# Kernel tuning notes

Measured on AMD Instinct MI355X. Metric: run time of the kernel, lower is better.

The kernel has to match this reference:

```python
import jax, jax.numpy as jnp
import numpy as np

N, E, F_IN, C, H = 50000, 800000, 256, 64, 2  # nodes, edges, in-feat, per-head dim, heads
NEG_SLOPE_ATT = 0.2   # GATConv leaky_relu slope
NEG_SLOPE = 0.01      # F.leaky_relu default
BN_EPS = 1e-5


def setup_inputs() -> dict:
    key = jax.random.key(0)
    ks = jax.random.split(key, 10)
    x = jax.random.normal(ks[0], (N, F_IN), dtype=jnp.float32)
    edge_index = jax.random.randint(ks[1], (2, E), 0, N, dtype=jnp.int32)
    # GATConv params
    W = jax.random.normal(ks[2], (F_IN, H * C), dtype=jnp.float32) / np.sqrt(F_IN)
    att_src = jax.random.normal(ks[3], (H, C), dtype=jnp.float32) / np.sqrt(C)
    att_dst = jax.random.normal(ks[4], (H, C), dtype=jnp.float32) / np.sqrt(C)
    conv_bias = jnp.zeros((H * C,), dtype=jnp.float32)
    # fc1: in = hidden*2*2 = 256, out = hidden = 64
    fc1_w = jax.random.normal(ks[5], (H * C * 2, C), dtype=jnp.float32) / np.sqrt(H * C * 2)
    fc1_b = jnp.zeros((C,), dtype=jnp.float32)
    bn_gamma = jnp.ones((C,), dtype=jnp.float32)
    bn_beta = jnp.zeros((C,), dtype=jnp.float32)
    bn_mean = jnp.zeros((C,), dtype=jnp.float32)
    bn_var = jnp.ones((C,), dtype=jnp.float32)
    fc2_w = jax.random.normal(ks[6], (C, 3), dtype=jnp.float32) / np.sqrt(C)
    fc2_b = jnp.zeros((3,), dtype=jnp.float32)
    return {"x": x, "edge_index": edge_index, "W": W, "att_src": att_src,
            "att_dst": att_dst, "conv_bias": conv_bias, "fc1_w": fc1_w, "fc1_b": fc1_b,
            "bn_gamma": bn_gamma, "bn_beta": bn_beta, "bn_mean": bn_mean,
            "bn_var": bn_var, "fc2_w": fc2_w, "fc2_b": fc2_b}


def gat_conv(x, edge_index, W, att_src, att_dst, bias):
    # Project: [N, H, C]
    h = (x @ W).reshape(N, H, C)
    a_s = jnp.einsum('nhc,hc->nh', h, att_src)  # [N, H]
    a_d = jnp.einsum('nhc,hc->nh', h, att_dst)
    # add self-loops (PyG default)
    loops = jnp.arange(N, dtype=edge_index.dtype)
    src = jnp.concatenate([edge_index[0], loops])
    dst = jnp.concatenate([edge_index[1], loops])
    e = jax.nn.leaky_relu(a_s[src] + a_d[dst], NEG_SLOPE_ATT)  # [E+N, H]
    # segment softmax over incoming edges of each dst node
    m = jax.ops.segment_max(e, dst, num_segments=N)
    e_exp = jnp.exp(e - m[dst])
    denom = jax.ops.segment_sum(e_exp, dst, num_segments=N)
    alpha = e_exp / denom[dst]  # [E+N, H]
    msg = h[src] * alpha[:, :, None]  # [E+N, H, C]
    out = jax.ops.segment_sum(msg, dst, num_segments=N)  # [N, H, C]
    return out.reshape(N, H * C) + bias


def reference(x, edge_index, W, att_src, att_dst, conv_bias, fc1_w, fc1_b,
              bn_gamma, bn_beta, bn_mean, bn_var, fc2_w, fc2_b):
    # eval mode: dropout = identity, BN uses running stats
    h = gat_conv(x, edge_index, W, att_src, att_dst, conv_bias)
    h = jax.nn.leaky_relu(h, NEG_SLOPE)
    edge_rep = jnp.concatenate([h[edge_index[0]], h[edge_index[1]]], axis=1)  # [E, 256]
    y = edge_rep @ fc1_w + fc1_b
    y = (y - bn_mean) * jax.lax.rsqrt(bn_var + BN_EPS) * bn_gamma + bn_beta
    y = jax.nn.leaky_relu(y, NEG_SLOPE)
    return y @ fc2_w + fc2_b  # [E, 3]
```

## Files before the change

### kernel.cpp

```cpp
#include <hip/hip_runtime.h>
#include <hip/hip_bf16.h>

#define N_NODES 50000
#define N_EDGES 800000
#define F_IN    256
#define C_DIM   64
#define HC      128
#define NPG     6250
#define NBB     32
#define NBLK    196
#define XW_BLOCKS   3125
#define HIST_BLOCKS 256

typedef __attribute__((ext_vector_type(8))) short bf16x8;
typedef __attribute__((ext_vector_type(4))) float f32x4;

static constexpr size_t OFF_HBF   = 0;
static constexpr size_t OFF_H2    = 12800000;
static constexpr size_t OFF_AB    = 25600000;
static constexpr size_t OFF_AS    = 38400000;
static constexpr size_t OFF_AD    = 38800000;
static constexpr size_t OFF_OFFS  = 39200000;
static constexpr size_t OFF_TOT   = 39400064;
static constexpr size_t OFF_PART  = 39800064;
static constexpr size_t OFF_CSR2  = 39801088;
static constexpr size_t OFF_WT    = 46201088;
static constexpr size_t OFF_FC1T  = 46266624;
static constexpr size_t OFF_SCALE = 46299392;
static constexpr size_t OFF_CC    = 46299904;
static constexpr size_t OFF_FC2M  = 46300416;
static constexpr size_t OFF_BCNT  = 46302464;
static constexpr size_t OFF_BASE  = 52702464;

__device__ __forceinline__ float2 bf2(unsigned u) {
    float2 r;
    r.x = __uint_as_float(u << 16);
    r.y = __uint_as_float(u & 0xffff0000u);
    return r;
}
__device__ __forceinline__ unsigned short f2bf(float f) {
    unsigned u = __float_as_uint(f);
    return (unsigned short)((u + 0x7fffu + ((u >> 16) & 1u)) >> 16);
}
__device__ __forceinline__ short f2bf_s(float f) {
    __hip_bfloat16 h = __float2bfloat16(f);
    return *reinterpret_cast<short*>(&h);
}

__global__ __launch_bounds__(256) void k_prep(const float* __restrict__ W,
                                              const float* __restrict__ fc1,
                                              const float* __restrict__ fc1_b,
                                              const float* __restrict__ gamma,
                                              const float* __restrict__ beta,
                                              const float* __restrict__ mean,
                                              const float* __restrict__ var,
                                              const float* __restrict__ fc2_w,
                                              unsigned short* __restrict__ Wt,
                                              unsigned short* __restrict__ fc1t,
                                              float* __restrict__ scale,
                                              float* __restrict__ cc,
                                              unsigned short* __restrict__ fc2m) {
    int id = blockIdx.x * 256 + threadIdx.x;
    if (id < 32768) {
        int n = id >> 8, k = id & 255;
        Wt[id] = f2bf(W[k * HC + n]);
    }
    int id2 = id - 32768;
    if (id2 >= 0 && id2 < 16384) {
        int j = id2 >> 7, q = id2 & 127;
        int L = q >> 1, b = q & 1;
        int kch = 32 * (L >> 4) + (L & 15) + 16 * b;
        float v = (j < 64) ? fc1[kch * 64 + j] : fc1[(128 + kch) * 64 + (j - 64)];
        fc1t[id2] = f2bf(v);
    }
    int id3 = id - (32768 + 16384);
    if (id3 >= 0 && id3 < 128) {
        int jj = id3 & 63;
        float s = gamma[jj] * rsqrtf(var[jj] + 1e-5f);
        scale[id3] = s;
        cc[id3] = (id3 < 64) ? 0.f : (fc1_b[jj] - mean[jj]) * s + beta[jj];
    }
    int id4 = id - (32768 + 16384 + 128);
    if (id4 >= 0 && id4 < 1024) {
        int kk = id4 >> 9, rem = id4 & 511;
        int lane = rem >> 3, j = rem & 7;
        int q  = kk * 16 + (lane >> 4) * 4 + (j >> 1);
        int ch = 32 * (q >> 4) + (q & 15) + 16 * (j & 1);
        int col = lane & 15;
        float v = (col < 3) ? fc2_w[ch * 3 + col] : 0.f;
        fc2m[id4] = f2bf(v);
    }
}

__global__ __launch_bounds__(256, 4) void k_front(const float* __restrict__ x,
                                                  const unsigned short* __restrict__ Wt,
                                                  const float* __restrict__ att_src,
                                                  const float* __restrict__ att_dst,
                                                  unsigned* __restrict__ h_p,
                                                  float* __restrict__ as_,
                                                  float* __restrict__ ad_,
                                                  const int* __restrict__ dst,
                                                  int* __restrict__ bcnt) {
    __shared__ int smem[6464];
    const int t = threadIdx.x;

    if (blockIdx.x < HIST_BLOCKS) {
        int* hist = smem;
        const int bid = blockIdx.x;
        const int g  = bid & 7;
        const int bi = bid >> 3;
        const int lo = g * NPG, hi = lo + NPG;
        for (int j = t; j < NPG; j += 256) hist[j] = 0;
        __syncthreads();
        const int4* d4 = (const int4*)dst + bi * 6250;
#pragma unroll 1
        for (int it = 0; it < 25; ++it) {
            int idx = it * 256 + t;
            if (idx < 6250) {
                int4 d = d4[idx];
                if (d.x >= lo && d.x < hi) atomicAdd(&hist[d.x - lo], 1);
                if (d.y >= lo && d.y < hi) atomicAdd(&hist[d.y - lo], 1);
                if (d.z >= lo && d.z < hi) atomicAdd(&hist[d.z - lo], 1);
                if (d.w >= lo && d.w < hi) atomicAdd(&hist[d.w - lo], 1);
            }
        }
        __syncthreads();
        int* row = bcnt + (size_t)(g * NBB + bi) * NPG;
        for (int j = t; j < NPG; j += 256) row[j] = hist[j];
        return;
    }

    float* xs  = (float*)smem;
    float* sAs = (float*)(smem + 4096);
    float* sAd = sAs + 32;
    const int v    = t >> 6;
    const int lane = t & 63;
    const int c16  = lane & 15;
    const int kg   = lane >> 4;
    const int r0   = (blockIdx.x - HIST_BLOCKS) * 16;
    if (t < 32) { sAs[t] = 0.f; sAd[t] = 0.f; }
    {
        const float4* xsrc = (const float4*)(x + (size_t)r0 * F_IN);
        float4* xsl = (float4*)xs;
#pragma unroll
        for (int it = 0; it < 4; ++it) {
            int cidx = it * 256 + t;
            int rl = cidx >> 6, j = cidx & 63;
            float4 val = xsrc[cidx];
            xsl[rl * 64 + (j ^ rl)] = val;
        }
    }
    const int cf0 = 2 * v, cf1 = 2 * v + 1;
    bf16x8 wf0[8], wf1[8];
#pragma unroll
    for (int kk = 0; kk < 8; ++kk) {
        wf0[kk] = *(const bf16x8*)(Wt + (size_t)(cf0 * 16 + c16) * 256 + kk * 32 + kg * 8);
        wf1[kk] = *(const bf16x8*)(Wt + (size_t)(cf1 * 16 + c16) * 256 + kk * 32 + kg * 8);
    }
    __syncthreads();

    f32x4 acc0 = {}, acc1 = {};
#pragma unroll
    for (int kk = 0; kk < 8; ++kk) {
        int j0 = kk * 8 + kg * 2;
        float4 a0 = *(const float4*)(xs + (size_t)(c16 * 64 + (j0 ^ c16)) * 4);
        float4 a1 = *(const float4*)(xs + (size_t)(c16 * 64 + ((j0 + 1) ^ c16)) * 4);
        float fv[8] = {a0.x, a0.y, a0.z, a0.w, a1.x, a1.y, a1.z, a1.w};
        bf16x8 ahi, alo;
#pragma unroll
        for (int q = 0; q < 8; ++q) {
            unsigned u = __float_as_uint(fv[q]);
            float hval = __uint_as_float(u & 0xffff0000u);
            float d = fv[q] - hval;
            ahi[q] = (short)(u >> 16);
            alo[q] = (short)(__float_as_uint(d) >> 16);
        }
        acc0 = __builtin_amdgcn_mfma_f32_16x16x32_bf16(alo, wf0[kk], acc0, 0, 0, 0);
        acc0 = __builtin_amdgcn_mfma_f32_16x16x32_bf16(ahi, wf0[kk], acc0, 0, 0, 0);
        acc1 = __builtin_amdgcn_mfma_f32_16x16x32_bf16(alo, wf1[kk], acc1, 0, 0, 0);
        acc1 = __builtin_amdgcn_mfma_f32_16x16x32_bf16(ahi, wf1[kk], acc1, 0, 0, 0);
    }
#pragma unroll
    for (int i = 0; i < 4; ++i) {
        int row = r0 + kg * 4 + i;
        unsigned pu = (unsigned)f2bf(acc0[i]) | ((unsigned)f2bf(acc1[i]) << 16);
        h_p[(size_t)row * 64 + v * 16 + c16] = pu;
    }
    float ws0 = att_src[cf0 * 16 + c16], ws1 = att_src[cf1 * 16 + c16];
    float wd0 = att_dst[cf0 * 16 + c16], wd1 = att_dst[cf1 * 16 + c16];
    float pas[4], pad[4];
#pragma unroll
    for (int i = 0; i < 4; ++i) {
        pas[i] = acc0[i] * ws0 + acc1[i] * ws1;
        pad[i] = acc0[i] * wd0 + acc1[i] * wd1;
    }
#pragma unroll
    for (int m = 1; m < 16; m <<= 1) {
#pragma unroll
        for (int i = 0; i < 4; ++i) {
            pas[i] += __shfl_xor(pas[i], m, 64);
            pad[i] += __shfl_xor(pad[i], m, 64);
        }
    }
    const int head = v >> 1;
    if (c16 == 0) {
#pragma unroll
        for (int i = 0; i < 4; ++i) {
            atomicAdd(&sAs[(kg * 4 + i) * 2 + head], pas[i]);
            atomicAdd(&sAd[(kg * 4 + i) * 2 + head], pad[i]);
        }
    }
    __syncthreads();
    if (t < 32) {
        int row = t >> 1, hd = t & 1;
        as_[(r0 + row) * 2 + hd] = sAs[row * 2 + hd];
        ad_[(r0 + row) * 2 + hd] = sAd[row * 2 + hd];
    }
}

__global__ void k_tot_part(const int* __restrict__ bcnt, int* __restrict__ tot,
                           int* __restrict__ part) {
    __shared__ int sd[256];
    int n = blockIdx.x * 256 + threadIdx.x;
    int s = 0;
    if (n < N_NODES) {
        int g = n / NPG, ln = n - g * NPG;
        const int* col = bcnt + (size_t)g * NBB * NPG + ln;
#pragma unroll
        for (int bi = 0; bi < NBB; ++bi) s += col[bi * NPG];
        tot[n] = s;
    }
    sd[threadIdx.x] = s;
    __syncthreads();
    for (int off = 128; off > 0; off >>= 1) {
        if (threadIdx.x < off) sd[threadIdx.x] += sd[threadIdx.x + off];
        __syncthreads();
    }
    if (threadIdx.x == 0) part[blockIdx.x] = sd[0];
}

__global__ void k_scan_base(const int* __restrict__ tot, const int* __restrict__ part,
                            const int* __restrict__ bcnt, int* __restrict__ offs,
                            int* __restrict__ base) {
    __shared__ int sp[256];
    __shared__ int sd[256];
    const int t = threadIdx.x;
    int pv = (t < NBLK && t < (int)blockIdx.x) ? part[t] : 0;
    sp[t] = pv;
    __syncthreads();
    for (int off = 128; off > 0; off >>= 1) {
        if (t < off) sp[t] += sp[t + off];
        __syncthreads();
    }
    const int bb = sp[0];
    __syncthreads();
    int i = blockIdx.x * 256 + t;
    int v = (i < N_NODES) ? tot[i] : 0;
    sd[t] = v;
    __syncthreads();
    for (int off = 1; off < 256; off <<= 1) {
        int u = (t >= off) ? sd[t - off] : 0;
        __syncthreads();
        sd[t] += u;
        __syncthreads();
    }
    if (i < N_NODES) {
        int o = bb + sd[t] - v;
        offs[i] = o;
        if (i == N_NODES - 1) offs[N_NODES] = o + v;
        int g = i / NPG, ln = i - g * NPG;
        const int* col = bcnt + (size_t)g * NBB * NPG + ln;
        int* bcol = base + (size_t)g * NBB * NPG + ln;
        int run = o;
#pragma unroll
        for (int bi = 0; bi < NBB; ++bi) {
            bcol[bi * NPG] = run;
            run += col[bi * NPG];
        }
    }
}

__global__ __launch_bounds__(256) void k_scatter(const int* __restrict__ src,
                                                 const int* __restrict__ dst,
                                                 const int* __restrict__ base,
                                                 int2* __restrict__ csr2) {
    __shared__ int cnt[NPG];
    const int g  = blockIdx.x & 7;
    const int bi = blockIdx.x >> 3;
    const int lo = g * NPG, hi = lo + NPG;
    const int* brow = base + (size_t)(g * NBB + bi) * NPG;
    for (int j = threadIdx.x; j < NPG; j += 256) cnt[j] = brow[j];
    __syncthreads();
    const int4* d4 = (const int4*)dst + bi * 6250;
    const int4* s4 = (const int4*)src + bi * 6250;
    const int ebase = bi * 25000;
#pragma unroll 1
    for (int it = 0; it < 25; ++it) {
        int idx = it * 256 + threadIdx.x;
        if (idx < 6250) {
            int4 d = d4[idx];
            int4 s = s4[idx];
            int e = ebase + idx * 4;
            if (d.x >= lo && d.x < hi) { int p = atomicAdd(&cnt[d.x - lo], 1); csr2[p] = make_int2(s.x, e);     }
            if (d.y >= lo && d.y < hi) { int p = atomicAdd(&cnt[d.y - lo], 1); csr2[p] = make_int2(s.y, e + 1); }
            if (d.z >= lo && d.z < hi) { int p = atomicAdd(&cnt[d.z - lo], 1); csr2[p] = make_int2(s.z, e + 2); }
            if (d.w >= lo && d.w < hi) { int p = atomicAdd(&cnt[d.w - lo], 1); csr2[p] = make_int2(s.w, e + 3); }
        }
    }
}

__global__ __launch_bounds__(256) void k_agg(const unsigned* __restrict__ h_p,
                                             const float* __restrict__ as_,
                                             const float* __restrict__ ad_,
                                             const int* __restrict__ offs,
                                             const int2* __restrict__ csr2,
                                             const float* __restrict__ conv_bias,
                                             unsigned* __restrict__ h2_p) {
    const int n    = blockIdx.x * 4 + (threadIdx.x >> 6);
    const int lane = threadIdx.x & 63;
    const int ql   = lane & 15;
    const int q    = lane >> 4;
    const int hd   = ql >> 3;
    const float adn = ad_[n * 2 + hd];
    const uint4* h4 = (const uint4*)h_p;
    float a[8] = {};
    float accw = 0.f;
    const int beg = offs[n], end = offs[n + 1];
    int i = beg + q;
    for (; i + 4 < end; i += 8) {
        int s0 = csr2[i].x;
        int s1 = csr2[i + 4].x;
        uint4 u0 = h4[(unsigned)(s0 * 16 + ql)];
        uint4 u1 = h4[(unsigned)(s1 * 16 + ql)];
        float l0 = as_[s0 * 2 + hd] + adn;
        float l1 = as_[s1 * 2 + hd] + adn;
        l0 = fmaxf(l0, 0.2f * l0);
        l1 = fmaxf(l1, 0.2f * l1);
        float w0 = __expf(l0), w1 = __expf(l1);
        float2 t;
        t = bf2(u0.x); a[0] += w0 * t.x; a[1] += w0 * t.y;
        t = bf2(u0.y); a[2] += w0 * t.x; a[3] += w0 * t.y;
        t = bf2(u0.z); a[4] += w0 * t.x; a[5] += w0 * t.y;
        t = bf2(u0.w); a[6] += w0 * t.x; a[7] += w0 * t.y;
        t = bf2(u1.x); a[0] += w1 * t.x; a[1] += w1 * t.y;
        t = bf2(u1.y); a[2] += w1 * t.x; a[3] += w1 * t.y;
        t = bf2(u1.z); a[4] += w1 * t.x; a[5] += w1 * t.y;
        t = bf2(u1.w); a[6] += w1 * t.x; a[7] += w1 * t.y;
        accw += w0 + w1;
    }
    if (i < end) {
        int s0 = csr2[i].x;
        uint4 u0 = h4[(unsigned)(s0 * 16 + ql)];
        float l0 = as_[s0 * 2 + hd] + adn;
        l0 = fmaxf(l0, 0.2f * l0);
        float w0 = __expf(l0);
        float2 t;
        t = bf2(u0.x); a[0] += w0 * t.x; a[1] += w0 * t.y;
        t = bf2(u0.y); a[2] += w0 * t.x; a[3] += w0 * t.y;
        t = bf2(u0.z); a[4] += w0 * t.x; a[5] += w0 * t.y;
        t = bf2(u0.w); a[6] += w0 * t.x; a[7] += w0 * t.y;
        accw += w0;
    }
#pragma unroll
    for (int m = 16; m < 64; m <<= 1) {
#pragma unroll
        for (int j = 0; j < 8; ++j) a[j] += __shfl_xor(a[j], m, 64);
        accw += __shfl_xor(accw, m, 64);
    }
    if (q == 0) {
        float es = as_[n * 2 + hd] + adn;
        es = fmaxf(es, 0.2f * es);
        float wsl = __expf(es);
        uint4 un = h4[(unsigned)(n * 16 + ql)];
        float2 t;
        t = bf2(un.x); a[0] += wsl * t.x; a[1] += wsl * t.y;
        t = bf2(un.y); a[2] += wsl * t.x; a[3] += wsl * t.y;
        t = bf2(un.z); a[4] += wsl * t.x; a[5] += wsl * t.y;
        t = bf2(un.w); a[6] += wsl * t.x; a[7] += wsl * t.y;
        accw += wsl;
        float rinv = 1.f / accw;
        unsigned pw[4];
#pragma unroll
        for (int j = 0; j < 4; ++j) {
            int w = 4 * ql + j;
            int c = 32 * (w >> 4) + (w & 15);
            float o0 = a[2 * j] * rinv + conv_bias[c];
            float o1 = a[2 * j + 1] * rinv + conv_bias[c + 16];
            o0 = fmaxf(o0, 0.01f * o0);
            o1 = fmaxf(o1, 0.01f * o1);
            pw[j] = (unsigned)f2bf(o0) | ((unsigned)f2bf(o1) << 16);
        }
        ((uint4*)h2_p)[(unsigned)(n * 16 + ql)] = make_uint4(pw[0], pw[1], pw[2], pw[3]);
    }
}

__global__ __launch_bounds__(256) void k_mfma_uv(const unsigned short* __restrict__ h2,
                                                 const unsigned short* __restrict__ fc1t,
                                                 const float* __restrict__ scale,
                                                 const float* __restrict__ cc,
                                                 unsigned* __restrict__ ab_p) {
    const int w = blockIdx.x * 4 + (threadIdx.x >> 6);
    if (w >= N_NODES / 16) return;
    const int lane = threadIdx.x & 63;
    const int c16  = lane & 15;
    const int kg   = lane >> 4;
    const int r0   = w * 16;
    const unsigned short* arow = h2 + (size_t)(r0 + c16) * HC + kg * 8;
    bf16x8 af[4];
#pragma unroll
    for (int kk = 0; kk < 4; ++kk) af[kk] = *(const bf16x8*)(arow + kk * 32);
    f32x4 acc[8] = {};
#pragma unroll
    for (int kk = 0; kk < 4; ++kk) {
        const unsigned short* wp = fc1t + c16 * HC + kk * 32 + kg * 8;
#pragma unroll
        for (int cf = 0; cf < 8; ++cf) {
            bf16x8 b = *(const bf16x8*)(wp + cf * 16 * HC);
            acc[cf] = __builtin_amdgcn_mfma_f32_16x16x32_bf16(af[kk], b, acc[cf], 0, 0, 0);
        }
    }
#pragma unroll
    for (int cf = 0; cf < 8; cf += 2) {
        int j0 = cf * 16 + c16, j1 = j0 + 16;
        float s0 = scale[j0], s1 = scale[j1];
        float q0 = cc[j0],    q1 = cc[j1];
#pragma unroll
        for (int i = 0; i < 4; ++i) {
            int row = r0 + kg * 4 + i;
            unsigned pu = (unsigned)f2bf(acc[cf][i] * s0 + q0)
                        | ((unsigned)f2bf(acc[cf + 1][i] * s1 + q1) << 16);
            ab_p[(size_t)row * 64 + (cf >> 1) * 16 + c16] = pu;
        }
    }
}

__device__ __forceinline__ void mk_afrag(uint4 ua, const float* bb, bf16x8& ap) {
    float2 t; float z;
    t = bf2(ua.x);
    z = t.x + bb[0]; z = fmaxf(z, 0.01f * z); ap[0] = f2bf_s(z);
    z = t.y + bb[1]; z = fmaxf(z, 0.01f * z); ap[1] = f2bf_s(z);
    t = bf2(ua.y);
    z = t.x + bb[2]; z = fmaxf(z, 0.01f * z); ap[2] = f2bf_s(z);
    z = t.y + bb[3]; z = fmaxf(z, 0.01f * z); ap[3] = f2bf_s(z);
    t = bf2(ua.z);
    z = t.x + bb[4]; z = fmaxf(z, 0.01f * z); ap[4] = f2bf_s(z);
    z = t.y + bb[5]; z = fmaxf(z, 0.01f * z); ap[5] = f2bf_s(z);
    t = bf2(ua.w);
    z = t.x + bb[6]; z = fmaxf(z, 0.01f * z); ap[6] = f2bf_s(z);
    z = t.y + bb[7]; z = fmaxf(z, 0.01f * z); ap[7] = f2bf_s(z);
}

__global__ __launch_bounds__(256) void k_edge(const int* __restrict__ offs,
                                              const int2* __restrict__ csr2,
                                              const unsigned* __restrict__ ab_p,
                                              const unsigned short* __restrict__ fc2m,
                                              const float* __restrict__ fc2_b,
                                              float* __restrict__ out) {
    const int n    = blockIdx.x * 4 + (threadIdx.x >> 6);
    const int lane = threadIdx.x & 63;
    const int c16  = lane & 15;
    const int kg   = lane >> 4;
    bf16x8 bfr0 = *(const bf16x8*)(fc2m + (size_t)lane * 8);
    bf16x8 bfr1 = *(const bf16x8*)(fc2m + (size_t)(64 + lane) * 8);
    const uint4* abv = (const uint4*)ab_p;
    uint4 ub0 = abv[(unsigned)(n * 16 + 8 + kg)];
    uint4 ub1 = abv[(unsigned)(n * 16 + 12 + kg)];
    float bb0[8], bb1[8];
    {
        float2 t;
        t = bf2(ub0.x); bb0[0] = t.x; bb0[1] = t.y;
        t = bf2(ub0.y); bb0[2] = t.x; bb0[3] = t.y;
        t = bf2(ub0.z); bb0[4] = t.x; bb0[5] = t.y;
        t = bf2(ub0.w); bb0[6] = t.x; bb0[7] = t.y;
        t = bf2(ub1.x); bb1[0] = t.x; bb1[1] = t.y;
        t = bf2(ub1.y); bb1[2] = t.x; bb1[3] = t.y;
        t = bf2(ub1.z); bb1[4] = t.x; bb1[5] = t.y;
        t = bf2(ub1.w); bb1[6] = t.x; bb1[7] = t.y;
    }
    const float ob = (c16 < 3) ? fc2_b[c16] : 0.f;
    const int beg = offs[n], end = offs[n + 1];
    for (int base = beg; base < end; base += 16) {
        int slot = base + c16;
        int2 ce = (slot < end) ? csr2[slot] : make_int2(0, 0);
        uint4 ua0 = abv[(unsigned)(ce.x * 16 + kg)];
        uint4 ua1 = abv[(unsigned)(ce.x * 16 + 4 + kg)];
        bf16x8 ap0, ap1;
        mk_afrag(ua0, bb0, ap0);
        mk_afrag(ua1, bb1, ap1);
        f32x4 acc = {};
        acc = __builtin_amdgcn_mfma_f32_16x16x32_bf16(ap0, bfr0, acc, 0, 0, 0);
        acc = __builtin_amdgcn_mfma_f32_16x16x32_bf16(ap1, bfr1, acc, 0, 0, 0);
#pragma unroll
        for (int i = 0; i < 4; ++i) {
            int eid = __shfl(ce.y, kg * 4 + i, 64);
            if (c16 < 3 && (base + kg * 4 + i) < end)
                out[(size_t)eid * 3 + c16] = acc[i] + ob;
        }
    }
}

extern "C" void kernel_launch(void* const* d_in, const int* in_sizes, int n_in,
                              void* d_out, int out_size, void* d_ws, size_t ws_size,
                              hipStream_t stream) {
    const float* x        = (const float*)d_in[0];
    const int*   ei       = (const int*)d_in[1];
    const float* W        = (const float*)d_in[2];
    const float* att_src  = (const float*)d_in[3];
    const float* att_dst  = (const float*)d_in[4];
    const float* conv_b   = (const float*)d_in[5];
    const float* fc1_w    = (const float*)d_in[6];
    const float* fc1_b    = (const float*)d_in[7];
    const float* gamma    = (const float*)d_in[8];
    const float* beta     = (const float*)d_in[9];
    const float* mean     = (const float*)d_in[10];
    const float* var      = (const float*)d_in[11];
    const float* fc2_w    = (const float*)d_in[12];
    const float* fc2_b    = (const float*)d_in[13];
    float*       out      = (float*)d_out;
    char*        ws       = (char*)d_ws;

    const int* src = ei;
    const int* dst = ei + N_EDGES;

    unsigned*       h_p   = (unsigned*)(ws + OFF_HBF);
    unsigned*       h2_p  = (unsigned*)(ws + OFF_H2);
    unsigned*       ab_p  = (unsigned*)(ws + OFF_AB);
    float*          as_   = (float*)(ws + OFF_AS);
    float*          ad_   = (float*)(ws + OFF_AD);
    int*            offs  = (int*)(ws + OFF_OFFS);
    int*            tot   = (int*)(ws + OFF_TOT);
    int*            part  = (int*)(ws + OFF_PART);
    int2*           csr2  = (int2*)(ws + OFF_CSR2);
    unsigned short* Wt    = (unsigned short*)(ws + OFF_WT);
    unsigned short* fc1t  = (unsigned short*)(ws + OFF_FC1T);
    float*          scale = (float*)(ws + OFF_SCALE);
    float*          cc    = (float*)(ws + OFF_CC);
    unsigned short* fc2m  = (unsigned short*)(ws + OFF_FC2M);
    int*            bcnt  = (int*)(ws + OFF_BCNT);
    int*            base  = (int*)(ws + OFF_BASE);

    k_prep<<<235, 256, 0, stream>>>(W, fc1_w, fc1_b, gamma, beta, mean, var, fc2_w,
                                    Wt, fc1t, scale, cc, fc2m);

    k_front<<<HIST_BLOCKS + XW_BLOCKS, 256, 0, stream>>>(x, Wt, att_src, att_dst,
                                                         h_p, as_, ad_, dst, bcnt);

    k_tot_part <<<NBLK, 256, 0, stream>>>(bcnt, tot, part);
    k_scan_base<<<NBLK, 256, 0, stream>>>(tot, part, bcnt, offs, base);
    k_scatter  <<<8 * NBB, 256, 0, stream>>>(src, dst, base, csr2);

    k_agg    <<<N_NODES / 4, 256, 0, stream>>>(h_p, as_, ad_, offs, csr2, conv_b, h2_p);
    k_mfma_uv<<<(N_NODES / 16 + 3) / 4, 256, 0, stream>>>((const unsigned short*)h2_p, fc1t, scale, cc, ab_p);
    k_edge   <<<N_NODES / 4, 256, 0, stream>>>(offs, csr2, ab_p, fc2m, fc2_b, out);
}
```

Measured before the change: 157.7 us.

## Fuse GAT aggregation with fc1 MFMA projection through shared memory

Merges the aggregation kernel and the per-node fc1 MFMA kernel into one. Each block now handles 16 nodes, four per wavefront processed sequentially, and stages the activated bf16 rows in LDS. After a barrier, each wave computes two 16-column MFMA tiles of the projection. This drops the h2 global round-trip and one launch, but each block gets 4x more serial gather work and a __syncthreads, which lowers parallelism and latency hiding in the gather phase.

```diff
diff --git a/kernel.cpp b/kernel.cpp
--- a/kernel.cpp
+++ b/kernel.cpp
@@ -16,7 +16,6 @@
 typedef __attribute__((ext_vector_type(4))) float f32x4;
 
 static constexpr size_t OFF_HBF   = 0;
-static constexpr size_t OFF_H2    = 12800000;
 static constexpr size_t OFF_AB    = 25600000;
 static constexpr size_t OFF_AS    = 38400000;
 static constexpr size_t OFF_AD    = 38800000;
@@ -309,128 +308,127 @@
     }
 }
 
-__global__ __launch_bounds__(256) void k_agg(const unsigned* __restrict__ h_p,
-                                             const float* __restrict__ as_,
-                                             const float* __restrict__ ad_,
-                                             const int* __restrict__ offs,
-                                             const int2* __restrict__ csr2,
-                                             const float* __restrict__ conv_bias,
-                                             unsigned* __restrict__ h2_p) {
-    const int n    = blockIdx.x * 4 + (threadIdx.x >> 6);
-    const int lane = threadIdx.x & 63;
+__global__ __launch_bounds__(256) void k_agg_uv(const unsigned* __restrict__ h_p,
+                                                const float* __restrict__ as_,
+                                                const float* __restrict__ ad_,
+                                                const int* __restrict__ offs,
+                                                const int2* __restrict__ csr2,
+                                                const float* __restrict__ conv_bias,
+                                                const unsigned short* __restrict__ fc1t,
+                                                const float* __restrict__ scale,
+                                                const float* __restrict__ cc,
+                                                unsigned* __restrict__ ab_p) {
+    __shared__ unsigned lds_h2[16 * 68];
+    const int t    = threadIdx.x;
+    const int v    = t >> 6;
+    const int lane = t & 63;
     const int ql   = lane & 15;
     const int q    = lane >> 4;
     const int hd   = ql >> 3;
-    const float adn = ad_[n * 2 + hd];
+    const int nbase = blockIdx.x * 16;
     const uint4* h4 = (const uint4*)h_p;
-    float a[8] = {};
-    float accw = 0.f;
-    const int beg = offs[n], end = offs[n + 1];
-    int i = beg + q;
-    for (; i + 4 < end; i += 8) {
-        int s0 = csr2[i].x;
-        int s1 = csr2[i + 4].x;
-        uint4 u0 = h4[(unsigned)(s0 * 16 + ql)];
-        uint4 u1 = h4[(unsigned)(s1 * 16 + ql)];
-        float l0 = as_[s0 * 2 + hd] + adn;
-        float l1 = as_[s1 * 2 + hd] + adn;
-        l0 = fmaxf(l0, 0.2f * l0);
-        l1 = fmaxf(l1, 0.2f * l1);
-        float w0 = __expf(l0), w1 = __expf(l1);
-        float2 t;
-        t = bf2(u0.x); a[0] += w0 * t.x; a[1] += w0 * t.y;
-        t = bf2(u0.y); a[2] += w0 * t.x; a[3] += w0 * t.y;
-        t = bf2(u0.z); a[4] += w0 * t.x; a[5] += w0 * t.y;
-        t = bf2(u0.w); a[6] += w0 * t.x; a[7] += w0 * t.y;
-        t = bf2(u1.x); a[0] += w1 * t.x; a[1] += w1 * t.y;
-        t = bf2(u1.y); a[2] += w1 * t.x; a[3] += w1 * t.y;
-        t = bf2(u1.z); a[4] += w1 * t.x; a[5] += w1 * t.y;
-        t = bf2(u1.w); a[6] += w1 * t.x; a[7] += w1 * t.y;
-        accw += w0 + w1;
-    }
-    if (i < end) {
-        int s0 = csr2[i].x;
-        uint4 u0 = h4[(unsigned)(s0 * 16 + ql)];
-        float l0 = as_[s0 * 2 + hd] + adn;
-        l0 = fmaxf(l0, 0.2f * l0);
-        float w0 = __expf(l0);
-        float2 t;
-        t = bf2(u0.x); a[0] += w0 * t.x; a[1] += w0 * t.y;
-        t = bf2(u0.y); a[2] += w0 * t.x; a[3] += w0 * t.y;
-        t = bf2(u0.z); a[4] += w0 * t.x; a[5] += w0 * t.y;
-        t = bf2(u0.w); a[6] += w0 * t.x; a[7] += w0 * t.y;
-        accw += w0;
-    }
-#pragma unroll
-    for (int m = 16; m < 64; m <<= 1) {
-#pragma unroll
-        for (int j = 0; j < 8; ++j) a[j] += __shfl_xor(a[j], m, 64);
-        accw += __shfl_xor(accw, m, 64);
-    }
-    if (q == 0) {
-        float es = as_[n * 2 + hd] + adn;
-        es = fmaxf(es, 0.2f * es);
-        float wsl = __expf(es);
-        uint4 un = h4[(unsigned)(n * 16 + ql)];
-        float2 t;
-        t = bf2(un.x); a[0] += wsl * t.x; a[1] += wsl * t.y;
-        t = bf2(un.y); a[2] += wsl * t.x; a[3] += wsl * t.y;
-        t = bf2(un.z); a[4] += wsl * t.x; a[5] += wsl * t.y;
-        t = bf2(un.w); a[6] += wsl * t.x; a[7] += wsl * t.y;
-        accw += wsl;
-        float rinv = 1.f / accw;
-        unsigned pw[4];
-#pragma unroll
-        for (int j = 0; j < 4; ++j) {
-            int w = 4 * ql + j;
-            int c = 32 * (w >> 4) + (w & 15);
-            float o0 = a[2 * j] * rinv + conv_bias[c];
-            float o1 = a[2 * j + 1] * rinv + conv_bias[c + 16];
-            o0 = fmaxf(o0, 0.01f * o0);
-            o1 = fmaxf(o1, 0.01f * o1);
-            pw[j] = (unsigned)f2bf(o0) | ((unsigned)f2bf(o1) << 16);
-        }
-        ((uint4*)h2_p)[(unsigned)(n * 16 + ql)] = make_uint4(pw[0], pw[1], pw[2], pw[3]);
-    }
-}
-
-__global__ __launch_bounds__(256) void k_mfma_uv(const unsigned short* __restrict__ h2,
-                                                 const unsigned short* __restrict__ fc1t,
-                                                 const float* __restrict__ scale,
-                                                 const float* __restrict__ cc,
-                                                 unsigned* __restrict__ ab_p) {
-    const int w = blockIdx.x * 4 + (threadIdx.x >> 6);
-    if (w >= N_NODES / 16) return;
-    const int lane = threadIdx.x & 63;
-    const int c16  = lane & 15;
-    const int kg   = lane >> 4;
-    const int r0   = w * 16;
-    const unsigned short* arow = h2 + (size_t)(r0 + c16) * HC + kg * 8;
+
+#pragma unroll 1
+    for (int j = 0; j < 4; ++j) {
+        const int ln = v * 4 + j;
+        const int n  = nbase + ln;
+        const float adn = ad_[n * 2 + hd];
+        float a[8] = {};
+        float accw = 0.f;
+        const int beg = offs[n], end = offs[n + 1];
+        int i = beg + q;
+        for (; i + 4 < end; i += 8) {
+            int s0 = csr2[i].x;
+            int s1 = csr2[i + 4].x;
+            uint4 u0 = h4[(unsigned)(s0 * 16 + ql)];
+            uint4 u1 = h4[(unsigned)(s1 * 16 + ql)];
+            float l0 = as_[s0 * 2 + hd] + adn;
+            float l1 = as_[s1 * 2 + hd] + adn;
+            l0 = fmaxf(l0, 0.2f * l0);
+            l1 = fmaxf(l1, 0.2f * l1);
+            float w0 = __expf(l0), w1 = __expf(l1);
+            float2 tt;
+            tt = bf2(u0.x); a[0] += w0 * tt.x; a[1] += w0 * tt.y;
+            tt = bf2(u0.y); a[2] += w0 * tt.x; a[3] += w0 * tt.y;
+            tt = bf2(u0.z); a[4] += w0 * tt.x; a[5] += w0 * tt.y;
+            tt = bf2(u0.w); a[6] += w0 * tt.x; a[7] += w0 * tt.y;
+            tt = bf2(u1.x); a[0] += w1 * tt.x; a[1] += w1 * tt.y;
+            tt = bf2(u1.y); a[2] += w1 * tt.x; a[3] += w1 * tt.y;
+            tt = bf2(u1.z); a[4] += w1 * tt.x; a[5] += w1 * tt.y;
+            tt = bf2(u1.w); a[6] += w1 * tt.x; a[7] += w1 * tt.y;
+            accw += w0 + w1;
+        }
+        if (i < end) {
+            int s0 = csr2[i].x;
+            uint4 u0 = h4[(unsigned)(s0 * 16 + ql)];
+            float l0 = as_[s0 * 2 + hd] + adn;
+            l0 = fmaxf(l0, 0.2f * l0);
+            float w0 = __expf(l0);
+            float2 tt;
+            tt = bf2(u0.x); a[0] += w0 * tt.x; a[1] += w0 * tt.y;
+            tt = bf2(u0.y); a[2] += w0 * tt.x; a[3] += w0 * tt.y;
+            tt = bf2(u0.z); a[4] += w0 * tt.x; a[5] += w0 * tt.y;
+            tt = bf2(u0.w); a[6] += w0 * tt.x; a[7] += w0 * tt.y;
+            accw += w0;
+        }
+#pragma unroll
+        for (int m = 16; m < 64; m <<= 1) {
+#pragma unroll
+            for (int jj = 0; jj < 8; ++jj) a[jj] += __shfl_xor(a[jj], m, 64);
+            accw += __shfl_xor(accw, m, 64);
+        }
+        if (q == 0) {
+            float es = as_[n * 2 + hd] + adn;
+            es = fmaxf(es, 0.2f * es);
+            float wsl = __expf(es);
+            uint4 un = h4[(unsigned)(n * 16 + ql)];
+            float2 tt;
+            tt = bf2(un.x); a[0] += wsl * tt.x; a[1] += wsl * tt.y;
+            tt = bf2(un.y); a[2] += wsl * tt.x; a[3] += wsl * tt.y;
+            tt = bf2(un.z); a[4] += wsl * tt.x; a[5] += wsl * tt.y;
+            tt = bf2(un.w); a[6] += wsl * tt.x; a[7] += wsl * tt.y;
+            accw += wsl;
+            float rinv = 1.f / accw;
+            unsigned pw[4];
+#pragma unroll
+            for (int jj = 0; jj < 4; ++jj) {
+                int w = 4 * ql + jj;
+                int c = 32 * (w >> 4) + (w & 15);
+                float o0 = a[2 * jj] * rinv + conv_bias[c];
+                float o1 = a[2 * jj + 1] * rinv + conv_bias[c + 16];
+                o0 = fmaxf(o0, 0.01f * o0);
+                o1 = fmaxf(o1, 0.01f * o1);
+                pw[jj] = (unsigned)f2bf(o0) | ((unsigned)f2bf(o1) << 16);
+            }
+            *(uint4*)&lds_h2[ln * 68 + ql * 4] = make_uint4(pw[0], pw[1], pw[2], pw[3]);
+        }
+    }
+    __syncthreads();
+
+    const int c16 = lane & 15;
+    const int kg  = lane >> 4;
+    const int cf0 = 2 * v, cf1 = 2 * v + 1;
     bf16x8 af[4];
 #pragma unroll
-    for (int kk = 0; kk < 4; ++kk) af[kk] = *(const bf16x8*)(arow + kk * 32);
-    f32x4 acc[8] = {};
+    for (int kk = 0; kk < 4; ++kk)
+        af[kk] = *(const bf16x8*)&lds_h2[c16 * 68 + kk * 16 + kg * 4];
+    f32x4 acc0 = {}, acc1 = {};
 #pragma unroll
     for (int kk = 0; kk < 4; ++kk) {
-        const unsigned short* wp = fc1t + c16 * HC + kk * 32 + kg * 8;
-#pragma unroll
-        for (int cf = 0; cf < 8; ++cf) {
-            bf16x8 b = *(const bf16x8*)(wp + cf * 16 * HC);
-            acc[cf] = __builtin_amdgcn_mfma_f32_16x16x32_bf16(af[kk], b, acc[cf], 0, 0, 0);
-        }
-    }
-#pragma unroll
-    for (int cf = 0; cf < 8; cf += 2) {
-        int j0 = cf * 16 + c16, j1 = j0 + 16;
-        float s0 = scale[j0], s1 = scale[j1];
-        float q0 = cc[j0],    q1 = cc[j1];
-#pragma unroll
-        for (int i = 0; i < 4; ++i) {
-            int row = r0 + kg * 4 + i;
-            unsigned pu = (unsigned)f2bf(acc[cf][i] * s0 + q0)
-                        | ((unsigned)f2bf(acc[cf + 1][i] * s1 + q1) << 16);
-            ab_p[(size_t)row * 64 + (cf >> 1) * 16 + c16] = pu;
-        }
+        bf16x8 b0 = *(const bf16x8*)(fc1t + (size_t)(cf0 * 16 + c16) * HC + kk * 32 + kg * 8);
+        bf16x8 b1 = *(const bf16x8*)(fc1t + (size_t)(cf1 * 16 + c16) * HC + kk * 32 + kg * 8);
+        acc0 = __builtin_amdgcn_mfma_f32_16x16x32_bf16(af[kk], b0, acc0, 0, 0, 0);
+        acc1 = __builtin_amdgcn_mfma_f32_16x16x32_bf16(af[kk], b1, acc1, 0, 0, 0);
+    }
+    const int j0 = cf0 * 16 + c16, j1 = j0 + 16;
+    const float s0 = scale[j0], s1 = scale[j1];
+    const float q0 = cc[j0],    q1 = cc[j1];
+#pragma unroll
+    for (int i = 0; i < 4; ++i) {
+        int row = nbase + kg * 4 + i;
+        unsigned pu = (unsigned)f2bf(acc0[i] * s0 + q0)
+                    | ((unsigned)f2bf(acc1[i] * s1 + q1) << 16);
+        ab_p[(size_t)row * 64 + v * 16 + c16] = pu;
     }
 }
 
@@ -523,7 +521,6 @@
     const int* dst = ei + N_EDGES;
 
     unsigned*       h_p   = (unsigned*)(ws + OFF_HBF);
-    unsigned*       h2_p  = (unsigned*)(ws + OFF_H2);
     unsigned*       ab_p  = (unsigned*)(ws + OFF_AB);
     float*          as_   = (float*)(ws + OFF_AS);
     float*          ad_   = (float*)(ws + OFF_AD);
@@ -549,7 +546,7 @@
     k_scan_base<<<NBLK, 256, 0, stream>>>(tot, part, bcnt, offs, base);
     k_scatter  <<<8 * NBB, 256, 0, stream>>>(src, dst, base, csr2);
 
-    k_agg    <<<N_NODES / 4, 256, 0, stream>>>(h_p, as_, ad_, offs, csr2, conv_b, h2_p);
-    k_mfma_uv<<<(N_NODES / 16 + 3) / 4, 256, 0, stream>>>((const unsigned short*)h2_p, fc1t, scale, cc, ab_p);
-    k_edge   <<<N_NODES / 4, 256, 0, stream>>>(offs, csr2, ab_p, fc2m, fc2_b, out);
-}
+    k_agg_uv<<<N_NODES / 16, 256, 0, stream>>>(h_p, as_, ad_, offs, csr2, conv_b,
+                                               fc1t, scale, cc, ab_p);
+    k_edge  <<<N_NODES / 4, 256, 0, stream>>>(offs, csr2, ab_p, fc2m, fc2_b, out);
+}
```

After: 151.6 us. 3.9% less time.
